# Kernel tuning notes

Measured on AMD Instinct MI355X. Metric: run time of the kernel, lower is better.

The kernel has to match this reference:

```python
import jax, jax.numpy as jnp
import numpy as np

IN_DIM = 256
HID = 256
A = 32          # n_agents
NH = 4          # attention heads
HD = 16         # head_dim = attention_dim / heads
CV = 16         # comm_value_dim
TOPK = 8
NACT = 20
BS = 2048
NEG = -1e10


def _lin(key, out_d, in_d):
    k1, k2 = jax.random.split(key)
    s = 1.0 / np.sqrt(in_d)
    w = jax.random.uniform(k1, (out_d, in_d), jnp.float32, -s, s)
    b = jax.random.uniform(k2, (out_d,), jnp.float32, -s, s)
    return w, b


def setup_inputs() -> dict:
    key = jax.random.key(0)
    ks = jax.random.split(key, 12)
    inputs = jax.random.normal(ks[0], (BS * A, IN_DIM), jnp.float32)
    hidden_state = jax.random.normal(ks[1], (BS * A, HID), jnp.float32)
    fc1_w, fc1_b = _lin(ks[2], HID, IN_DIM)
    gru_w_ih, gru_b_ih = _lin(ks[3], 3 * HID, HID)
    gru_w_hh, gru_b_hh = _lin(ks[4], 3 * HID, HID)
    q_w, q_b = _lin(ks[5], NH * HD, HID)
    k_w, k_b = _lin(ks[6], NH * HD, HID)
    v_w, v_b = _lin(ks[7], NH * CV, HID)
    g_w, g_b = _lin(ks[8], NH, HID)
    p1_w, p1_b = _lin(ks[9], HID, HID + NH * CV)
    p2_w, p2_b = _lin(ks[10], NACT, HID)
    return {
        'inputs': inputs, 'hidden_state': hidden_state,
        'fc1_w': fc1_w, 'fc1_b': fc1_b,
        'gru_w_ih': gru_w_ih, 'gru_w_hh': gru_w_hh,
        'gru_b_ih': gru_b_ih, 'gru_b_hh': gru_b_hh,
        'q_w': q_w, 'q_b': q_b, 'k_w': k_w, 'k_b': k_b,
        'v_w': v_w, 'v_b': v_b, 'g_w': g_w, 'g_b': g_b,
        'p1_w': p1_w, 'p1_b': p1_b, 'p2_w': p2_w, 'p2_b': p2_b,
        'bs': BS,
    }


def _forward(inputs, hidden_state, fc1_w, fc1_b, gru_w_ih, gru_w_hh,
             gru_b_ih, gru_b_hh, q_w, q_b, k_w, k_b, v_w, v_b,
             g_w, g_b, p1_w, p1_b, p2_w, p2_b, bs):
    x = jax.nn.relu(inputs @ fc1_w.T + fc1_b)
    h_in = hidden_state.reshape(-1, HID)
    # torch GRUCell: gates ordered r, z, n
    gi = x @ gru_w_ih.T + gru_b_ih
    gh = h_in @ gru_w_hh.T + gru_b_hh
    gi_r, gi_z, gi_n = jnp.split(gi, 3, axis=-1)
    gh_r, gh_z, gh_n = jnp.split(gh, 3, axis=-1)
    r = jax.nn.sigmoid(gi_r + gh_r)
    z = jax.nn.sigmoid(gi_z + gh_z)
    n = jnp.tanh(gi_n + r * gh_n)
    h = (1.0 - z) * n + z * h_in

    ah = h.reshape(bs, A, HID)                      # agent_hidden
    q = (ah @ q_w.T + q_b).reshape(bs, A, NH, HD)
    k = (ah @ k_w.T + k_b).reshape(bs, A, NH, HD)
    v = (ah @ v_w.T + v_b).reshape(bs, A, NH, CV)

    scores = jnp.einsum('bqhd,bkhd->bqkh', q, k) / np.sqrt(HD)  # [bs,A,A,NH]
    eye = jnp.eye(A, dtype=bool)[None, :, :, None]
    scores = jnp.where(eye, NEG, scores)

    # topk mask along neighbor dim (k < A-1 so mask is applied)
    sp = scores.transpose(0, 1, 3, 2)               # [bs,A,NH,A]
    _, idx = jax.lax.top_k(sp, TOPK)
    keep = jax.nn.one_hot(idx, A, dtype=jnp.float32).sum(axis=-2) > 0
    sp = jnp.where(keep, sp, NEG)
    sparse_scores = sp.transpose(0, 1, 3, 2)        # [bs,A,A,NH]

    alpha = jax.nn.softmax(sparse_scores, axis=2)
    head_messages = jnp.einsum('bqkh,bkhv->bqhv', alpha, v)  # [bs,A,NH,CV]
    gates = jax.nn.sigmoid(ah @ g_w.T + g_b)[..., None]      # [bs,A,NH,1]
    gated = head_messages * gates

    policy_in = jnp.concatenate([ah, gated.reshape(bs, A, NH * CV)], axis=-1)
    policy_in = policy_in.reshape(bs * A, HID + NH * CV)
    logits = jax.nn.relu(policy_in @ p1_w.T + p1_b) @ p2_w.T + p2_b
    return logits, h


def reference(inputs, hidden_state, fc1_w, fc1_b, gru_w_ih, gru_w_hh,
              gru_b_ih, gru_b_hh, q_w, q_b, k_w, k_b, v_w, v_b,
              g_w, g_b, p1_w, p1_b, p2_w, p2_b, bs):
    return _forward(inputs, hidden_state, fc1_w, fc1_b, gru_w_ih, gru_w_hh,
                    gru_b_ih, gru_b_hh, q_w, q_b, k_w, k_b, v_w, v_b,
                    g_w, g_b, p1_w, p1_b, p2_w, p2_b, bs)
```

## Files before the change

### kernel.cpp

```cpp
#include <hip/hip_runtime.h>
#include <hip/hip_bf16.h>
#include <math.h>

#define NBATCH 2048
#define NAG 32
#define HIDD 256
#define INDIM 256
#define PIN 320
#define NACTN 20
#define NEGV -1e10f
#define MT 64
#define NROWS (NBATCH*NAG)

typedef __attribute__((ext_vector_type(8))) __bf16 bf16x8;
typedef __attribute__((ext_vector_type(4))) float f32x4;

#define WO_W1   0
#define WO_WIH  65536
#define WO_WHH  262144
#define WO_WQ   458752
#define WO_WK   475136
#define WO_WV   491520
#define WO_WG   507904
#define WO_WP1  508928
#define WO_WP2  590848
#define WSO_Q   1048576
#define WSO_K   (WSO_Q + NROWS*64)
#define WSO_V   (WSO_K + NROWS*64)
#define WSO_G   (WSO_V + NROWS*64)
#define WSO_MSG (WSO_G + NROWS*4)

__device__ __forceinline__ unsigned short f2bf(float f) {
    union { float f; unsigned int i; } x; x.f = f;
    unsigned int r = x.i + 0x7fffu + ((x.i >> 16) & 1u);
    return (unsigned short)(r >> 16);
}
__device__ __forceinline__ float bf2f(unsigned short u) {
    union { unsigned int i; float f; } x; x.i = ((unsigned int)u) << 16; return x.f;
}
__device__ __forceinline__ float sigm(float x) { return 1.0f / (1.0f + __expf(-x)); }

__device__ __forceinline__ int swz(int row, int col) {
    return row*256 + ((((col >> 3)) ^ (row & 7)) << 3) + (col & 7);
}
__device__ __forceinline__ int swzf(int row, int frag) {
    return row*256 + ((frag ^ (row & 7)) << 3);
}
__device__ __forceinline__ int swzf64(int row, int frag) {
    return row*64 + ((frag ^ (row & 7)) << 3);
}

__device__ __forceinline__ bf16x8 ldfrag(const unsigned short* p) {
    return *(const bf16x8*)(const void*)p;
}
union ZU { uint4 u; bf16x8 v; };
__device__ __forceinline__ bf16x8 zfrag() {
    ZU x; x.u = make_uint4(0u, 0u, 0u, 0u); return x.v;
}
#define MFMA(a,b,c) __builtin_amdgcn_mfma_f32_16x16x32_bf16(a,b,c,0,0,0)

__global__ void __launch_bounds__(256)
convert_weights(const float* __restrict__ W1,  const float* __restrict__ Wih,
                const float* __restrict__ Whh, const float* __restrict__ Wq,
                const float* __restrict__ Wk,  const float* __restrict__ Wv,
                const float* __restrict__ Wg,  const float* __restrict__ Wp1,
                const float* __restrict__ Wp2, unsigned short* __restrict__ dst)
{
    int b = (int)blockIdx.x;
    const float* src; int base;
    if      (b <  64) { src = W1;  base = WO_W1;              }
    else if (b < 256) { src = Wih; base = WO_WIH; b -=  64;   }
    else if (b < 448) { src = Whh; base = WO_WHH; b -= 256;   }
    else if (b < 464) { src = Wq;  base = WO_WQ;  b -= 448;   }
    else if (b < 480) { src = Wk;  base = WO_WK;  b -= 464;   }
    else if (b < 496) { src = Wv;  base = WO_WV;  b -= 480;   }
    else if (b < 497) { src = Wg;  base = WO_WG;  b -= 496;   }
    else if (b < 577) { src = Wp1; base = WO_WP1; b -= 497;   }
    else              { src = Wp2; base = WO_WP2; b -= 577;   }
    const int idx = b * 1024 + (int)threadIdx.x * 4;
    float4 v = *(const float4*)(const void*)(src + idx);
    ushort4 u;
    u.x = f2bf(v.x); u.y = f2bf(v.y); u.z = f2bf(v.z); u.w = f2bf(v.w);
    *(ushort4*)(void*)(dst + base + idx) = u;
}

__global__ void __launch_bounds__(256, 2)
k1_gru_qkvg(const float* __restrict__ gIn, const float* __restrict__ gH,
            const unsigned short* __restrict__ wsW,
            const float* __restrict__ B1,
            const float* __restrict__ Bih, const float* __restrict__ Bhh,
            const float* __restrict__ Bq,  const float* __restrict__ Bk,
            const float* __restrict__ Bv,  const float* __restrict__ Bg,
            float* __restrict__ outH,
            unsigned short* __restrict__ wsQ, unsigned short* __restrict__ wsK,
            unsigned short* __restrict__ wsV, unsigned short* __restrict__ wsG)
{
    __shared__ __align__(16) unsigned short lA[MT*256];
    __shared__ __align__(16) unsigned short lB[MT*256];

    const unsigned short* W1  = wsW + WO_W1;
    const unsigned short* Wih = wsW + WO_WIH;
    const unsigned short* Whh = wsW + WO_WHH;
    const unsigned short* Wq  = wsW + WO_WQ;
    const unsigned short* Wk  = wsW + WO_WK;
    const unsigned short* Wv  = wsW + WO_WV;
    const unsigned short* Wg  = wsW + WO_WG;

    const int tid  = (int)threadIdx.x;
    const int lane = tid & 63;
    const int wv   = tid >> 6;
    const int l15  = lane & 15;
    const int quad = lane >> 4;
    const long rowBase = (long)blockIdx.x * MT;

    #pragma unroll
    for (int i = 0; i < 16; ++i) {
        const int job  = i*256 + tid;
        const int frag = job & 31;
        const int row  = (job >> 5) & 63;
        const int buf  = job >> 11;
        const float* src = (buf ? gH : gIn) + (rowBase + row)*256 + frag*8;
        float4 v0 = *(const float4*)(const void*)(src);
        float4 v1 = *(const float4*)(const void*)(src + 4);
        uint4 pk;
        pk.x = ((unsigned int)f2bf(v0.y) << 16) | f2bf(v0.x);
        pk.y = ((unsigned int)f2bf(v0.w) << 16) | f2bf(v0.z);
        pk.z = ((unsigned int)f2bf(v1.y) << 16) | f2bf(v1.x);
        pk.w = ((unsigned int)f2bf(v1.w) << 16) | f2bf(v1.z);
        unsigned short* dst = buf ? lB : lA;
        *(uint4*)(void*)(dst + swzf(row, frag)) = pk;
    }
    __syncthreads();

    f32x4 xa[4][4];
    #pragma unroll
    for (int i4 = 0; i4 < 4; ++i4) {
        const int nt = i4*4 + wv;
        const int n  = nt*16 + l15;
        f32x4 a0 = {0.f,0.f,0.f,0.f}, a1 = {0.f,0.f,0.f,0.f};
        f32x4 a2 = {0.f,0.f,0.f,0.f}, a3 = {0.f,0.f,0.f,0.f};
        #pragma unroll
        for (int kt = 0; kt < 8; ++kt) {
            const int frag = kt*4 + quad;
            bf16x8 bw = ldfrag(W1 + n*INDIM + frag*8);
            a0 = MFMA(ldfrag(lA + swzf(     l15, frag)), bw, a0);
            a1 = MFMA(ldfrag(lA + swzf(16 + l15, frag)), bw, a1);
            a2 = MFMA(ldfrag(lA + swzf(32 + l15, frag)), bw, a2);
            a3 = MFMA(ldfrag(lA + swzf(48 + l15, frag)), bw, a3);
        }
        const float b = B1[n];
        #pragma unroll
        for (int r = 0; r < 4; ++r) {
            a0[r] = fmaxf(a0[r] + b, 0.f); a1[r] = fmaxf(a1[r] + b, 0.f);
            a2[r] = fmaxf(a2[r] + b, 0.f); a3[r] = fmaxf(a3[r] + b, 0.f);
        }
        xa[i4][0] = a0; xa[i4][1] = a1; xa[i4][2] = a2; xa[i4][3] = a3;
    }
    __syncthreads();
    #pragma unroll
    for (int i4 = 0; i4 < 4; ++i4) {
        const int nt = i4*4 + wv;
        #pragma unroll
        for (int m = 0; m < 4; ++m) {
            #pragma unroll
            for (int r = 0; r < 4; ++r)
                lA[swz(m*16 + quad*4 + r, nt*16 + l15)] = f2bf(xa[i4][m][r]);
        }
    }
    __syncthreads();

    for (int jt = wv; jt < 16; jt += 4) {
        const int n = jt*16 + l15;
        f32x4 ir[4], iz[4], in_[4], hr[4], hz[4], hn[4];
        #pragma unroll
        for (int m = 0; m < 4; ++m) {
            ir[m] = (f32x4){0.f,0.f,0.f,0.f}; iz[m] = (f32x4){0.f,0.f,0.f,0.f};
            in_[m]= (f32x4){0.f,0.f,0.f,0.f}; hr[m] = (f32x4){0.f,0.f,0.f,0.f};
            hz[m] = (f32x4){0.f,0.f,0.f,0.f}; hn[m] = (f32x4){0.f,0.f,0.f,0.f};
        }
        #pragma unroll 2
        for (int kt = 0; kt < 8; ++kt) {
            const int frag = kt*4 + quad;
            const int k0 = frag*8;
            bf16x8 ax[4], ah[4];
            #pragma unroll
            for (int m = 0; m < 4; ++m) {
                ax[m] = ldfrag(lA + swzf(m*16 + l15, frag));
                ah[m] = ldfrag(lB + swzf(m*16 + l15, frag));
            }
            bf16x8 br = ldfrag(Wih + (n      )*HIDD + k0);
            bf16x8 bz = ldfrag(Wih + (n + 256)*HIDD + k0);
            bf16x8 bn = ldfrag(Wih + (n + 512)*HIDD + k0);
            bf16x8 cr = ldfrag(Whh + (n      )*HIDD + k0);
            bf16x8 cz = ldfrag(Whh + (n + 256)*HIDD + k0);
            bf16x8 cn = ldfrag(Whh + (n + 512)*HIDD + k0);
            #pragma unroll
            for (int m = 0; m < 4; ++m) {
                ir[m] = MFMA(ax[m], br, ir[m]);
                iz[m] = MFMA(ax[m], bz, iz[m]);
                in_[m]= MFMA(ax[m], bn, in_[m]);
                hr[m] = MFMA(ah[m], cr, hr[m]);
                hz[m] = MFMA(ah[m], cz, hz[m]);
                hn[m] = MFMA(ah[m], cn, hn[m]);
            }
        }
        const float bir_ = Bih[n], biz_ = Bih[n+256], bin_ = Bih[n+512];
        const float bhr_ = Bhh[n], bhz_ = Bhh[n+256], bhn_ = Bhh[n+512];
        #pragma unroll
        for (int m = 0; m < 4; ++m) {
            #pragma unroll
            for (int r = 0; r < 4; ++r) {
                const int row = m*16 + quad*4 + r;
                const float hprev = bf2f(lB[swz(row, n)]);
                const float rr = sigm(ir[m][r] + bir_ + hr[m][r] + bhr_);
                const float zz = sigm(iz[m][r] + biz_ + hz[m][r] + bhz_);
                const float nn = tanhf(in_[m][r] + bin_ + rr*(hn[m][r] + bhn_));
                outH[(rowBase + row)*HIDD + n] = (1.0f - zz)*nn + zz*hprev;
            }
        }
    }
    __syncthreads();

    #pragma unroll
    for (int i = 0; i < 8; ++i) {
        const int job  = i*256 + tid;
        const int frag = job & 31;
        const int row  = job >> 5;
        const float* src = outH + (rowBase + row)*256 + frag*8;
        float4 v0 = *(const float4*)(const void*)(src);
        float4 v1 = *(const float4*)(const void*)(src + 4);
        uint4 pk;
        pk.x = ((unsigned int)f2bf(v0.y) << 16) | f2bf(v0.x);
        pk.y = ((unsigned int)f2bf(v0.w) << 16) | f2bf(v0.z);
        pk.z = ((unsigned int)f2bf(v1.y) << 16) | f2bf(v1.x);
        pk.w = ((unsigned int)f2bf(v1.w) << 16) | f2bf(v1.z);
        *(uint4*)(void*)(lA + swzf(row, frag)) = pk;
    }
    __syncthreads();

    for (int job = wv; job < 13; job += 4) {
        const unsigned short* W; const float* Bi; unsigned short* dst; int nb;
        if      (job < 4)  { W = Wq; Bi = Bq; dst = wsQ; nb = job;     }
        else if (job < 8)  { W = Wk; Bi = Bk; dst = wsK; nb = job - 4; }
        else if (job < 12) { W = Wv; Bi = Bv; dst = wsV; nb = job - 8; }
        else               { W = Wg; Bi = Bg; dst = wsG; nb = 0;       }
        const bool isg   = (job == 12);
        const bool valid = !isg || (l15 < 4);
        const int n = nb*16 + l15;
        f32x4 ac[4];
        #pragma unroll
        for (int m = 0; m < 4; ++m) ac[m] = (f32x4){0.f,0.f,0.f,0.f};
        #pragma unroll
        for (int kt = 0; kt < 8; ++kt) {
            const int frag = kt*4 + quad;
            bf16x8 bw = valid ? ldfrag(W + n*HIDD + frag*8) : zfrag();
            #pragma unroll
            for (int m = 0; m < 4; ++m)
                ac[m] = MFMA(ldfrag(lA + swzf(m*16 + l15, frag)), bw, ac[m]);
        }
        if (valid) {
            const float b = Bi[n];
            #pragma unroll
            for (int m = 0; m < 4; ++m) {
                #pragma unroll
                for (int r = 0; r < 4; ++r) {
                    const int row = m*16 + quad*4 + r;
                    const float v = ac[m][r] + b;
                    if (isg) dst[(rowBase + row)*4  + l15]          = f2bf(v);
                    else     dst[(rowBase + row)*64 + nb*16 + l15]  = f2bf(v);
                }
            }
        }
    }
}

#define QS 68
__global__ void __launch_bounds__(256, 4)
k2_attn(const unsigned short* __restrict__ wsQ, const unsigned short* __restrict__ wsK,
        const unsigned short* __restrict__ wsV, const unsigned short* __restrict__ wsG,
        unsigned short* __restrict__ wsM)
{
    __shared__ unsigned short sQ[2][32*QS];
    __shared__ unsigned short sK[2][32*QS];
    __shared__ unsigned short sV[2][32*QS];
    __shared__ unsigned short sG[2][32*4];

    const int tid = (int)threadIdx.x;
    const long b0 = (long)blockIdx.x * 2;

    #pragma unroll
    for (int i = 0; i < 12; ++i) {
        const int j  = i*256 + tid;
        const int b  = (j >= 1536) ? 1 : 0;
        const int jj = b ? (j - 1536) : j;
        const int mat = jj >> 9;
        const int e   = jj & 511;
        const int row = e >> 4, c4 = e & 15;
        const unsigned short* srcm = (mat == 0) ? wsQ : (mat == 1) ? wsK : wsV;
        unsigned short* dstm = (mat == 0) ? sQ[b] : (mat == 1) ? sK[b] : sV[b];
        *(ushort4*)(void*)(dstm + row*QS + c4*4) =
            *(const ushort4*)(const void*)(srcm + ((b0 + b)*32 + row)*64 + c4*4);
    }
    if (tid < 64) {
        const int b = tid >> 5, row = tid & 31;
        *(ushort4*)(void*)(sG[b] + row*4) =
            *(const ushort4*)(const void*)(wsG + ((b0 + b)*32 + row)*4);
    }
    __syncthreads();

    const int b  = tid >> 7;
    const int h  = (tid >> 5) & 3;
    const int qi = tid & 31;
    const unsigned short* q_ = sQ[b];
    const unsigned short* k_ = sK[b];
    const unsigned short* v_ = sV[b];

    float qv[16];
    #pragma unroll
    for (int c = 0; c < 16; ++c) qv[c] = bf2f(q_[qi*QS + h*16 + c]);
    float s0[32];
    #pragma unroll
    for (int ki = 0; ki < 32; ++ki) {
        float acc = 0.0f;
        #pragma unroll
        for (int c = 0; c < 16; ++c) acc += qv[c] * bf2f(k_[ki*QS + h*16 + c]);
        acc *= 0.25f;
        s0[ki] = (ki == qi) ? NEGV : acc;
    }
    unsigned int mask = 0u;
    float m1 = 0.0f;
    for (int t = 0; t < 8; ++t) {
        float best = -3.0e38f; int bidx = 0;
        #pragma unroll
        for (int i = 0; i < 32; ++i) {
            bool better = (((mask >> i) & 1u) == 0u) && (s0[i] > best);
            best = better ? s0[i] : best;
            bidx = better ? i : bidx;
        }
        mask |= (1u << bidx);
        if (t == 0) m1 = best;
    }
    float sum = 0.0f;
    #pragma unroll
    for (int i = 0; i < 32; ++i) {
        float v = ((mask >> i) & 1u) ? s0[i] : NEGV;
        sum += __expf(v - m1);
    }
    const float inv = 1.0f / sum;
    const float gate = sigm(bf2f(sG[b][qi*4 + h]));
    float msg[16];
    #pragma unroll
    for (int c = 0; c < 16; ++c) msg[c] = 0.0f;
    #pragma unroll
    for (int ki = 0; ki < 32; ++ki) {
        float v = ((mask >> ki) & 1u) ? s0[ki] : NEGV;
        float al = __expf(v - m1) * inv;
        #pragma unroll
        for (int c = 0; c < 16; ++c) msg[c] += al * bf2f(v_[ki*QS + h*16 + c]);
    }
    unsigned short mb[16];
    #pragma unroll
    for (int c = 0; c < 16; ++c) mb[c] = f2bf(msg[c] * gate);
    unsigned short* dst = wsM + ((b0 + b)*32 + qi)*64 + h*16;
    #pragma unroll
    for (int c4 = 0; c4 < 4; ++c4) {
        ushort4 u;
        u.x = mb[c4*4]; u.y = mb[c4*4+1]; u.z = mb[c4*4+2]; u.w = mb[c4*4+3];
        *(ushort4*)(void*)(dst + c4*4) = u;
    }
}

__global__ void __launch_bounds__(256, 3)
k3_policy(const float* __restrict__ gHnew, const unsigned short* __restrict__ wsW,
          const unsigned short* __restrict__ wsM,
          const float* __restrict__ Bp1, const float* __restrict__ Bp2,
          float* __restrict__ outL)
{
    __shared__ __align__(16) unsigned short lH[MT*256];
    __shared__ __align__(16) unsigned short lM[MT*64];

    const unsigned short* Wp1 = wsW + WO_WP1;
    const unsigned short* Wp2 = wsW + WO_WP2;

    const int tid  = (int)threadIdx.x;
    const int lane = tid & 63;
    const int wv   = tid >> 6;
    const int l15  = lane & 15;
    const int quad = lane >> 4;
    const long rowBase = (long)blockIdx.x * MT;

    #pragma unroll
    for (int i = 0; i < 8; ++i) {
        const int job  = i*256 + tid;
        const int frag = job & 31;
        const int row  = job >> 5;
        const float* src = gHnew + (rowBase + row)*256 + frag*8;
        float4 v0 = *(const float4*)(const void*)(src);
        float4 v1 = *(const float4*)(const void*)(src + 4);
        uint4 pk;
        pk.x = ((unsigned int)f2bf(v0.y) << 16) | f2bf(v0.x);
        pk.y = ((unsigned int)f2bf(v0.w) << 16) | f2bf(v0.z);
        pk.z = ((unsigned int)f2bf(v1.y) << 16) | f2bf(v1.x);
        pk.w = ((unsigned int)f2bf(v1.w) << 16) | f2bf(v1.z);
        *(uint4*)(void*)(lH + swzf(row, frag)) = pk;
    }
    #pragma unroll
    for (int i = 0; i < 2; ++i) {
        const int job  = i*256 + tid;
        const int frag = job & 7;
        const int row  = job >> 3;
        *(uint4*)(void*)(lM + swzf64(row, frag)) =
            *(const uint4*)(const void*)(wsM + (rowBase + row)*64 + frag*8);
    }
    __syncthreads();

    f32x4 pa[4][4];
    #pragma unroll
    for (int i4 = 0; i4 < 4; ++i4) {
        const int nt = i4*4 + wv;
        const int n  = nt*16 + l15;
        f32x4 a0 = {0.f,0.f,0.f,0.f}, a1 = {0.f,0.f,0.f,0.f};
        f32x4 a2 = {0.f,0.f,0.f,0.f}, a3 = {0.f,0.f,0.f,0.f};
        #pragma unroll
        for (int kt = 0; kt < 10; ++kt) {
            bf16x8 bw = ldfrag(Wp1 + n*PIN + kt*32 + quad*8);
            bf16x8 f0, f1, f2, f3;
            if (kt < 8) {
                const int frag = kt*4 + quad;
                f0 = ldfrag(lH + swzf(     l15, frag));
                f1 = ldfrag(lH + swzf(16 + l15, frag));
                f2 = ldfrag(lH + swzf(32 + l15, frag));
                f3 = ldfrag(lH + swzf(48 + l15, frag));
            } else {
                const int frag = (kt - 8)*4 + quad;
                f0 = ldfrag(lM + swzf64(     l15, frag));
                f1 = ldfrag(lM + swzf64(16 + l15, frag));
                f2 = ldfrag(lM + swzf64(32 + l15, frag));
                f3 = ldfrag(lM + swzf64(48 + l15, frag));
            }
            a0 = MFMA(f0, bw, a0); a1 = MFMA(f1, bw, a1);
            a2 = MFMA(f2, bw, a2); a3 = MFMA(f3, bw, a3);
        }
        const float b = Bp1[n];
        #pragma unroll
        for (int r = 0; r < 4; ++r) {
            a0[r] = fmaxf(a0[r] + b, 0.f); a1[r] = fmaxf(a1[r] + b, 0.f);
            a2[r] = fmaxf(a2[r] + b, 0.f); a3[r] = fmaxf(a3[r] + b, 0.f);
        }
        pa[i4][0] = a0; pa[i4][1] = a1; pa[i4][2] = a2; pa[i4][3] = a3;
    }
    __syncthreads();
    #pragma unroll
    for (int i4 = 0; i4 < 4; ++i4) {
        const int nt = i4*4 + wv;
        #pragma unroll
        for (int m = 0; m < 4; ++m) {
            #pragma unroll
            for (int r = 0; r < 4; ++r)
                lH[swz(m*16 + quad*4 + r, nt*16 + l15)] = f2bf(pa[i4][m][r]);
        }
    }
    __syncthreads();

    for (int j = wv; j < 8; j += 4) {
        const int ntile = j >> 2, m = j & 3;
        const int n = ntile*16 + l15;
        const bool valid = (n < NACTN);
        f32x4 ac = {0.f,0.f,0.f,0.f};
        #pragma unroll
        for (int kt = 0; kt < 8; ++kt) {
            const int frag = kt*4 + quad;
            bf16x8 bw = valid ? ldfrag(Wp2 + n*HIDD + frag*8) : zfrag();
            ac = MFMA(ldfrag(lH + swzf(m*16 + l15, frag)), bw, ac);
        }
        if (valid) {
            const float b = Bp2[n];
            #pragma unroll
            for (int r = 0; r < 4; ++r)
                outL[(rowBase + m*16 + quad*4 + r)*NACTN + n] = ac[r] + b;
        }
    }
}

extern "C" void kernel_launch(void* const* d_in, const int* in_sizes, int n_in,
                              void* d_out, int out_size, void* d_ws, size_t ws_size,
                              hipStream_t stream) {
    (void)in_sizes; (void)n_in; (void)ws_size; (void)out_size;
    const float* gIn = (const float*)d_in[0];
    const float* gH  = (const float*)d_in[1];
    const float* W1  = (const float*)d_in[2];
    const float* B1  = (const float*)d_in[3];
    const float* Wih = (const float*)d_in[4];
    const float* Whh = (const float*)d_in[5];
    const float* Bih = (const float*)d_in[6];
    const float* Bhh = (const float*)d_in[7];
    const float* Wq  = (const float*)d_in[8];
    const float* Bq  = (const float*)d_in[9];
    const float* Wk  = (const float*)d_in[10];
    const float* Bk  = (const float*)d_in[11];
    const float* Wv  = (const float*)d_in[12];
    const float* Bv  = (const float*)d_in[13];
    const float* Wg  = (const float*)d_in[14];
    const float* Bg  = (const float*)d_in[15];
    const float* Wp1 = (const float*)d_in[16];
    const float* Bp1 = (const float*)d_in[17];
    const float* Wp2 = (const float*)d_in[18];
    const float* Bp2 = (const float*)d_in[19];
    float* outL = (float*)d_out;
    float* outH = outL + (size_t)NBATCH * NAG * NACTN;
    unsigned short* wsW = (unsigned short*)d_ws;

    hipLaunchKernelGGL(convert_weights, dim3(582), dim3(256), 0, stream,
        W1, Wih, Whh, Wq, Wk, Wv, Wg, Wp1, Wp2, wsW);
    hipLaunchKernelGGL(k1_gru_qkvg, dim3(NROWS/MT), dim3(256), 0, stream,
        gIn, gH, wsW, B1, Bih, Bhh, Bq, Bk, Bv, Bg,
        outH, wsW + WSO_Q, wsW + WSO_K, wsW + WSO_V, wsW + WSO_G);
    hipLaunchKernelGGL(k2_attn, dim3(NBATCH/2), dim3(256), 0, stream,
        wsW + WSO_Q, wsW + WSO_K, wsW + WSO_V, wsW + WSO_G, wsW + WSO_MSG);
    hipLaunchKernelGGL(k3_policy, dim3(NROWS/MT), dim3(256), 0, stream,
        outH, wsW, wsW + WSO_MSG, Bp1, Bp2, outL);
}
```

Measured before the change: 414.2 us.

## Pre-convert hidden state to bf16 and restructure GRU kernel for higher occupancy

Adds a kernel that converts the incoming hidden state to bf16 in workspace. A new GRU kernel uses a single LDS buffer, reads the bf16 h_prev straight from global memory, and writes a bf16 copy of the new h for the policy kernel to load without conversion. This lets the GRU kernel target 4 blocks per CU instead of 2, and the policy kernel's occupancy hint is also raised. Separately, sigmoid and tanh now use a fast reciprocal, and the attention softmax caches its exponentials so they are not recomputed. The new path runs only when the workspace is large enough. It adds an extra pass over the hidden state plus additional workspace traffic.

```diff
diff --git a/kernel.cpp b/kernel.cpp
--- a/kernel.cpp
+++ b/kernel.cpp
@@ -29,6 +29,9 @@
 #define WSO_V   (WSO_K + NROWS*64)
 #define WSO_G   (WSO_V + NROWS*64)
 #define WSO_MSG (WSO_G + NROWS*4)
+#define WSO_H   (WSO_MSG + NROWS*64)
+#define WSO_HO  (WSO_H + NROWS*256)
+#define WS_NEED_BYTES ((size_t)(WSO_HO + (size_t)NROWS*256) * 2u)
 
 __device__ __forceinline__ unsigned short f2bf(float f) {
     union { float f; unsigned int i; } x; x.f = f;
@@ -38,7 +41,12 @@
 __device__ __forceinline__ float bf2f(unsigned short u) {
     union { unsigned int i; float f; } x; x.i = ((unsigned int)u) << 16; return x.f;
 }
-__device__ __forceinline__ float sigm(float x) { return 1.0f / (1.0f + __expf(-x)); }
+__device__ __forceinline__ float frcp(float x) { return __builtin_amdgcn_rcpf(x); }
+__device__ __forceinline__ float sigm(float x) { return frcp(1.0f + __expf(-x)); }
+__device__ __forceinline__ float tanh_fast(float x) {
+    float e = __expf(2.0f * x);
+    return 1.0f - 2.0f * frcp(e + 1.0f);
+}
 
 __device__ __forceinline__ int swz(int row, int col) {
     return row*256 + ((((col >> 3)) ^ (row & 7)) << 3) + (col & 7);
@@ -84,16 +92,223 @@
     *(ushort4*)(void*)(dst + base + idx) = u;
 }
 
+__global__ void __launch_bounds__(256)
+convert_h(const float* __restrict__ gH, unsigned short* __restrict__ wsHO)
+{
+    const long base = (long)blockIdx.x * 16384;
+    const int tid = (int)threadIdx.x;
+    #pragma unroll
+    for (int i = 0; i < 8; ++i) {
+        const long off = base + (long)(i*256 + tid) * 8;
+        float4 v0 = *(const float4*)(const void*)(gH + off);
+        float4 v1 = *(const float4*)(const void*)(gH + off + 4);
+        uint4 pk;
+        pk.x = ((unsigned int)f2bf(v0.y) << 16) | f2bf(v0.x);
+        pk.y = ((unsigned int)f2bf(v0.w) << 16) | f2bf(v0.z);
+        pk.z = ((unsigned int)f2bf(v1.y) << 16) | f2bf(v1.x);
+        pk.w = ((unsigned int)f2bf(v1.w) << 16) | f2bf(v1.z);
+        *(uint4*)(void*)(wsHO + off) = pk;
+    }
+}
+
+__global__ void __launch_bounds__(256, 4)
+k1_new(const float* __restrict__ gIn,
+       const unsigned short* __restrict__ wsW,
+       const unsigned short* __restrict__ wsHO,
+       const float* __restrict__ B1,
+       const float* __restrict__ Bih, const float* __restrict__ Bhh,
+       const float* __restrict__ Bq,  const float* __restrict__ Bk,
+       const float* __restrict__ Bv,  const float* __restrict__ Bg,
+       float* __restrict__ outH, unsigned short* __restrict__ wsH,
+       unsigned short* __restrict__ wsQ, unsigned short* __restrict__ wsK,
+       unsigned short* __restrict__ wsV, unsigned short* __restrict__ wsG)
+{
+    __shared__ __align__(16) unsigned short lA[MT*256];
+
+    const unsigned short* W1  = wsW + WO_W1;
+    const unsigned short* Wih = wsW + WO_WIH;
+    const unsigned short* Whh = wsW + WO_WHH;
+    const unsigned short* Wq  = wsW + WO_WQ;
+    const unsigned short* Wk  = wsW + WO_WK;
+    const unsigned short* Wv  = wsW + WO_WV;
+    const unsigned short* Wg  = wsW + WO_WG;
+
+    const int tid  = (int)threadIdx.x;
+    const int lane = tid & 63;
+    const int wv   = tid >> 6;
+    const int l15  = lane & 15;
+    const int quad = lane >> 4;
+    const long rowBase = (long)blockIdx.x * MT;
+
+    #pragma unroll
+    for (int i = 0; i < 8; ++i) {
+        const int job  = i*256 + tid;
+        const int frag = job & 31;
+        const int row  = job >> 5;
+        const float* src = gIn + (rowBase + row)*256 + frag*8;
+        float4 v0 = *(const float4*)(const void*)(src);
+        float4 v1 = *(const float4*)(const void*)(src + 4);
+        uint4 pk;
+        pk.x = ((unsigned int)f2bf(v0.y) << 16) | f2bf(v0.x);
+        pk.y = ((unsigned int)f2bf(v0.w) << 16) | f2bf(v0.z);
+        pk.z = ((unsigned int)f2bf(v1.y) << 16) | f2bf(v1.x);
+        pk.w = ((unsigned int)f2bf(v1.w) << 16) | f2bf(v1.z);
+        *(uint4*)(void*)(lA + swzf(row, frag)) = pk;
+    }
+    __syncthreads();
+
+    f32x4 xa[4][4];
+    #pragma unroll
+    for (int i4 = 0; i4 < 4; ++i4) {
+        const int nt = i4*4 + wv;
+        const int n  = nt*16 + l15;
+        f32x4 a0 = {0.f,0.f,0.f,0.f}, a1 = {0.f,0.f,0.f,0.f};
+        f32x4 a2 = {0.f,0.f,0.f,0.f}, a3 = {0.f,0.f,0.f,0.f};
+        #pragma unroll
+        for (int kt = 0; kt < 8; ++kt) {
+            const int frag = kt*4 + quad;
+            bf16x8 bw = ldfrag(W1 + n*INDIM + frag*8);
+            a0 = MFMA(ldfrag(lA + swzf(     l15, frag)), bw, a0);
+            a1 = MFMA(ldfrag(lA + swzf(16 + l15, frag)), bw, a1);
+            a2 = MFMA(ldfrag(lA + swzf(32 + l15, frag)), bw, a2);
+            a3 = MFMA(ldfrag(lA + swzf(48 + l15, frag)), bw, a3);
+        }
+        const float b = B1[n];
+        #pragma unroll
+        for (int r = 0; r < 4; ++r) {
+            a0[r] = fmaxf(a0[r] + b, 0.f); a1[r] = fmaxf(a1[r] + b, 0.f);
+            a2[r] = fmaxf(a2[r] + b, 0.f); a3[r] = fmaxf(a3[r] + b, 0.f);
+        }
+        xa[i4][0] = a0; xa[i4][1] = a1; xa[i4][2] = a2; xa[i4][3] = a3;
+    }
+    __syncthreads();
+    #pragma unroll
+    for (int i4 = 0; i4 < 4; ++i4) {
+        const int nt = i4*4 + wv;
+        #pragma unroll
+        for (int m = 0; m < 4; ++m) {
+            #pragma unroll
+            for (int r = 0; r < 4; ++r)
+                lA[swz(m*16 + quad*4 + r, nt*16 + l15)] = f2bf(xa[i4][m][r]);
+        }
+    }
+    __syncthreads();
+
+    for (int jt = wv; jt < 16; jt += 4) {
+        const int n = jt*16 + l15;
+        const float bir_ = Bih[n], biz_ = Bih[n+256], bin_ = Bih[n+512];
+        const float bhr_ = Bhh[n], bhz_ = Bhh[n+256], bhn_ = Bhh[n+512];
+        #pragma unroll
+        for (int half = 0; half < 2; ++half) {
+            const int r0 = half*32;
+            f32x4 ir0={0.f,0.f,0.f,0.f}, ir1={0.f,0.f,0.f,0.f};
+            f32x4 iz0={0.f,0.f,0.f,0.f}, iz1={0.f,0.f,0.f,0.f};
+            f32x4 in0={0.f,0.f,0.f,0.f}, in1={0.f,0.f,0.f,0.f};
+            f32x4 hr0={0.f,0.f,0.f,0.f}, hr1={0.f,0.f,0.f,0.f};
+            f32x4 hz0={0.f,0.f,0.f,0.f}, hz1={0.f,0.f,0.f,0.f};
+            f32x4 hn0={0.f,0.f,0.f,0.f}, hn1={0.f,0.f,0.f,0.f};
+            #pragma unroll 2
+            for (int kt = 0; kt < 8; ++kt) {
+                const int frag = kt*4 + quad;
+                const int k0 = frag*8;
+                bf16x8 ax0 = ldfrag(lA + swzf(r0 +      l15, frag));
+                bf16x8 ax1 = ldfrag(lA + swzf(r0 + 16 + l15, frag));
+                bf16x8 ah0 = ldfrag(wsHO + (rowBase + r0 +      l15)*256 + k0);
+                bf16x8 ah1 = ldfrag(wsHO + (rowBase + r0 + 16 + l15)*256 + k0);
+                bf16x8 br = ldfrag(Wih + (n      )*HIDD + k0);
+                bf16x8 bz = ldfrag(Wih + (n + 256)*HIDD + k0);
+                bf16x8 bn = ldfrag(Wih + (n + 512)*HIDD + k0);
+                bf16x8 cr = ldfrag(Whh + (n      )*HIDD + k0);
+                bf16x8 cz = ldfrag(Whh + (n + 256)*HIDD + k0);
+                bf16x8 cn = ldfrag(Whh + (n + 512)*HIDD + k0);
+                ir0 = MFMA(ax0, br, ir0); ir1 = MFMA(ax1, br, ir1);
+                iz0 = MFMA(ax0, bz, iz0); iz1 = MFMA(ax1, bz, iz1);
+                in0 = MFMA(ax0, bn, in0); in1 = MFMA(ax1, bn, in1);
+                hr0 = MFMA(ah0, cr, hr0); hr1 = MFMA(ah1, cr, hr1);
+                hz0 = MFMA(ah0, cz, hz0); hz1 = MFMA(ah1, cz, hz1);
+                hn0 = MFMA(ah0, cn, hn0); hn1 = MFMA(ah1, cn, hn1);
+            }
+            #pragma unroll
+            for (int mm = 0; mm < 2; ++mm) {
+                f32x4 gr = mm ? ir1 : ir0;
+                f32x4 gz = mm ? iz1 : iz0;
+                f32x4 gn = mm ? in1 : in0;
+                f32x4 hr_ = mm ? hr1 : hr0;
+                f32x4 hz_ = mm ? hz1 : hz0;
+                f32x4 hn_ = mm ? hn1 : hn0;
+                #pragma unroll
+                for (int r = 0; r < 4; ++r) {
+                    const int rw = r0 + mm*16 + quad*4 + r;
+                    const long go = (rowBase + rw)*256 + n;
+                    const float hprev = bf2f(wsHO[go]);
+                    const float rr = sigm(gr[r] + bir_ + hr_[r] + bhr_);
+                    const float zz = sigm(gz[r] + biz_ + hz_[r] + bhz_);
+                    const float nn = tanh_fast(gn[r] + bin_ + rr*(hn_[r] + bhn_));
+                    const float hv = (1.0f - zz)*nn + zz*hprev;
+                    outH[go] = hv;
+                    wsH[go]  = f2bf(hv);
+                }
+            }
+        }
+    }
+    __syncthreads();
+
+    #pragma unroll
+    for (int i = 0; i < 8; ++i) {
+        const int job  = i*256 + tid;
+        const int frag = job & 31;
+        const int row  = job >> 5;
+        *(uint4*)(void*)(lA + swzf(row, frag)) =
+            *(const uint4*)(const void*)(wsH + (rowBase + row)*256 + frag*8);
+    }
+    __syncthreads();
+
+    for (int job = wv; job < 13; job += 4) {
+        const unsigned short* W; const float* Bi; unsigned short* dst; int nb;
+        if      (job < 4)  { W = Wq; Bi = Bq; dst = wsQ; nb = job;     }
+        else if (job < 8)  { W = Wk; Bi = Bk; dst = wsK; nb = job - 4; }
+        else if (job < 12) { W = Wv; Bi = Bv; dst = wsV; nb = job - 8; }
+        else               { W = Wg; Bi = Bg; dst = wsG; nb = 0;       }
+        const bool isg   = (job == 12);
+        const bool valid = !isg || (l15 < 4);
+        const int n = nb*16 + l15;
+        f32x4 ac[4];
+        #pragma unroll
+        for (int m = 0; m < 4; ++m) ac[m] = (f32x4){0.f,0.f,0.f,0.f};
+        #pragma unroll
+        for (int kt = 0; kt < 8; ++kt) {
+            const int frag = kt*4 + quad;
+            bf16x8 bw = valid ? ldfrag(W + n*HIDD + frag*8) : zfrag();
+            #pragma unroll
+            for (int m = 0; m < 4; ++m)
+                ac[m] = MFMA(ldfrag(lA + swzf(m*16 + l15, frag)), bw, ac[m]);
+        }
+        if (valid) {
+            const float b = Bi[n];
+            #pragma unroll
+            for (int m = 0; m < 4; ++m) {
+                #pragma unroll
+                for (int r = 0; r < 4; ++r) {
+                    const int row = m*16 + quad*4 + r;
+                    const float v = ac[m][r] + b;
+                    if (isg) dst[(rowBase + row)*4  + l15]          = f2bf(v);
+                    else     dst[(rowBase + row)*64 + nb*16 + l15]  = f2bf(v);
+                }
+            }
+        }
+    }
+}
+
 __global__ void __launch_bounds__(256, 2)
-k1_gru_qkvg(const float* __restrict__ gIn, const float* __restrict__ gH,
-            const unsigned short* __restrict__ wsW,
-            const float* __restrict__ B1,
-            const float* __restrict__ Bih, const float* __restrict__ Bhh,
-            const float* __restrict__ Bq,  const float* __restrict__ Bk,
-            const float* __restrict__ Bv,  const float* __restrict__ Bg,
-            float* __restrict__ outH,
-            unsigned short* __restrict__ wsQ, unsigned short* __restrict__ wsK,
-            unsigned short* __restrict__ wsV, unsigned short* __restrict__ wsG)
+k1_fb(const float* __restrict__ gIn, const float* __restrict__ gH,
+      const unsigned short* __restrict__ wsW,
+      const float* __restrict__ B1,
+      const float* __restrict__ Bih, const float* __restrict__ Bhh,
+      const float* __restrict__ Bq,  const float* __restrict__ Bk,
+      const float* __restrict__ Bv,  const float* __restrict__ Bg,
+      float* __restrict__ outH,
+      unsigned short* __restrict__ wsQ, unsigned short* __restrict__ wsK,
+      unsigned short* __restrict__ wsV, unsigned short* __restrict__ wsG)
 {
     __shared__ __align__(16) unsigned short lA[MT*256];
     __shared__ __align__(16) unsigned short lB[MT*256];
@@ -214,7 +429,7 @@
                 const float hprev = bf2f(lB[swz(row, n)]);
                 const float rr = sigm(ir[m][r] + bir_ + hr[m][r] + bhr_);
                 const float zz = sigm(iz[m][r] + biz_ + hz[m][r] + bhz_);
-                const float nn = tanhf(in_[m][r] + bin_ + rr*(hn[m][r] + bhn_));
+                const float nn = tanh_fast(in_[m][r] + bin_ + rr*(hn[m][r] + bhn_));
                 outH[(rowBase + row)*HIDD + n] = (1.0f - zz)*nn + zz*hprev;
             }
         }
@@ -343,18 +558,18 @@
     float sum = 0.0f;
     #pragma unroll
     for (int i = 0; i < 32; ++i) {
-        float v = ((mask >> i) & 1u) ? s0[i] : NEGV;
-        sum += __expf(v - m1);
-    }
-    const float inv = 1.0f / sum;
+        const float e = ((mask >> i) & 1u) ? __expf(s0[i] - m1) : 0.0f;
+        s0[i] = e;
+        sum += e;
+    }
+    const float inv = frcp(sum);
     const float gate = sigm(bf2f(sG[b][qi*4 + h]));
     float msg[16];
     #pragma unroll
     for (int c = 0; c < 16; ++c) msg[c] = 0.0f;
     #pragma unroll
     for (int ki = 0; ki < 32; ++ki) {
-        float v = ((mask >> ki) & 1u) ? s0[ki] : NEGV;
-        float al = __expf(v - m1) * inv;
+        const float al = s0[ki] * inv;
         #pragma unroll
         for (int c = 0; c < 16; ++c) msg[c] += al * bf2f(v_[ki*QS + h*16 + c]);
     }
@@ -370,11 +585,11 @@
     }
 }
 
-__global__ void __launch_bounds__(256, 3)
+__global__ void __launch_bounds__(256, 4)
 k3_policy(const float* __restrict__ gHnew, const unsigned short* __restrict__ wsW,
-          const unsigned short* __restrict__ wsM,
+          const unsigned short* __restrict__ wsM, const unsigned short* __restrict__ wsH,
           const float* __restrict__ Bp1, const float* __restrict__ Bp2,
-          float* __restrict__ outL)
+          float* __restrict__ outL, int useH16)
 {
     __shared__ __align__(16) unsigned short lH[MT*256];
     __shared__ __align__(16) unsigned short lM[MT*64];
@@ -389,20 +604,31 @@
     const int quad = lane >> 4;
     const long rowBase = (long)blockIdx.x * MT;
 
-    #pragma unroll
-    for (int i = 0; i < 8; ++i) {
-        const int job  = i*256 + tid;
-        const int frag = job & 31;
-        const int row  = job >> 5;
-        const float* src = gHnew + (rowBase + row)*256 + frag*8;
-        float4 v0 = *(const float4*)(const void*)(src);
-        float4 v1 = *(const float4*)(const void*)(src + 4);
-        uint4 pk;
-        pk.x = ((unsigned int)f2bf(v0.y) << 16) | f2bf(v0.x);
-        pk.y = ((unsigned int)f2bf(v0.w) << 16) | f2bf(v0.z);
-        pk.z = ((unsigned int)f2bf(v1.y) << 16) | f2bf(v1.x);
-        pk.w = ((unsigned int)f2bf(v1.w) << 16) | f2bf(v1.z);
-        *(uint4*)(void*)(lH + swzf(row, frag)) = pk;
+    if (useH16) {
+        #pragma unroll
+        for (int i = 0; i < 8; ++i) {
+            const int job  = i*256 + tid;
+            const int frag = job & 31;
+            const int row  = job >> 5;
+            *(uint4*)(void*)(lH + swzf(row, frag)) =
+                *(const uint4*)(const void*)(wsH + (rowBase + row)*256 + frag*8);
+        }
+    } else {
+        #pragma unroll
+        for (int i = 0; i < 8; ++i) {
+            const int job  = i*256 + tid;
+            const int frag = job & 31;
+            const int row  = job >> 5;
+            const float* src = gHnew + (rowBase + row)*256 + frag*8;
+            float4 v0 = *(const float4*)(const void*)(src);
+            float4 v1 = *(const float4*)(const void*)(src + 4);
+            uint4 pk;
+            pk.x = ((unsigned int)f2bf(v0.y) << 16) | f2bf(v0.x);
+            pk.y = ((unsigned int)f2bf(v0.w) << 16) | f2bf(v0.z);
+            pk.z = ((unsigned int)f2bf(v1.y) << 16) | f2bf(v1.x);
+            pk.w = ((unsigned int)f2bf(v1.w) << 16) | f2bf(v1.z);
+            *(uint4*)(void*)(lH + swzf(row, frag)) = pk;
+        }
     }
     #pragma unroll
     for (int i = 0; i < 2; ++i) {
@@ -485,7 +711,7 @@
 extern "C" void kernel_launch(void* const* d_in, const int* in_sizes, int n_in,
                               void* d_out, int out_size, void* d_ws, size_t ws_size,
                               hipStream_t stream) {
-    (void)in_sizes; (void)n_in; (void)ws_size; (void)out_size;
+    (void)in_sizes; (void)n_in; (void)out_size;
     const float* gIn = (const float*)d_in[0];
     const float* gH  = (const float*)d_in[1];
     const float* W1  = (const float*)d_in[2];
@@ -510,13 +736,24 @@
     float* outH = outL + (size_t)NBATCH * NAG * NACTN;
     unsigned short* wsW = (unsigned short*)d_ws;
 
+    const int preconv = (ws_size >= WS_NEED_BYTES) ? 1 : 0;
+
     hipLaunchKernelGGL(convert_weights, dim3(582), dim3(256), 0, stream,
         W1, Wih, Whh, Wq, Wk, Wv, Wg, Wp1, Wp2, wsW);
-    hipLaunchKernelGGL(k1_gru_qkvg, dim3(NROWS/MT), dim3(256), 0, stream,
-        gIn, gH, wsW, B1, Bih, Bhh, Bq, Bk, Bv, Bg,
-        outH, wsW + WSO_Q, wsW + WSO_K, wsW + WSO_V, wsW + WSO_G);
+    if (preconv) {
+        hipLaunchKernelGGL(convert_h, dim3(1024), dim3(256), 0, stream,
+            gH, wsW + WSO_HO);
+        hipLaunchKernelGGL(k1_new, dim3(NROWS/MT), dim3(256), 0, stream,
+            gIn, wsW, wsW + WSO_HO, B1, Bih, Bhh, Bq, Bk, Bv, Bg,
+            outH, wsW + WSO_H,
+            wsW + WSO_Q, wsW + WSO_K, wsW + WSO_V, wsW + WSO_G);
+    } else {
+        hipLaunchKernelGGL(k1_fb, dim3(NROWS/MT), dim3(256), 0, stream,
+            gIn, gH, wsW, B1, Bih, Bhh, Bq, Bk, Bv, Bg,
+            outH, wsW + WSO_Q, wsW + WSO_K, wsW + WSO_V, wsW + WSO_G);
+    }
     hipLaunchKernelGGL(k2_attn, dim3(NBATCH/2), dim3(256), 0, stream,
         wsW + WSO_Q, wsW + WSO_K, wsW + WSO_V, wsW + WSO_G, wsW + WSO_MSG);
     hipLaunchKernelGGL(k3_policy, dim3(NROWS/MT), dim3(256), 0, stream,
-        outH, wsW, wsW + WSO_MSG, Bp1, Bp2, outL);
-}
+        outH, wsW, wsW + WSO_MSG, wsW + WSO_H, Bp1, Bp2, outL, preconv);
+}
```

Result: slower. 656.0 us (+58.4%).

## Fuse attention kernel into policy kernel and use fast sigmoid/tanh

Applied to the files above, without the earlier changes.

Merges the top-k sparse attention kernel into the policy MLP kernel. Each 64-row block now computes the gated messages for its two batches straight into shared memory, so the message workspace round trip through global memory and one launch go away. The hidden layer is written to a separate LDS buffer, which removes the register staging and the extra barrier. It also swaps in hardware reciprocal for sigmoid and an exp-based tanh in the GRU epilogue, at some cost in precision. Extra LDS use and a lower occupancy bound (2 blocks) are the tradeoff.

```diff
diff --git a/kernel.cpp b/kernel.cpp
--- a/kernel.cpp
+++ b/kernel.cpp
@@ -28,7 +28,6 @@
 #define WSO_K   (WSO_Q + NROWS*64)
 #define WSO_V   (WSO_K + NROWS*64)
 #define WSO_G   (WSO_V + NROWS*64)
-#define WSO_MSG (WSO_G + NROWS*4)
 
 __device__ __forceinline__ unsigned short f2bf(float f) {
     union { float f; unsigned int i; } x; x.f = f;
@@ -38,13 +37,21 @@
 __device__ __forceinline__ float bf2f(unsigned short u) {
     union { unsigned int i; float f; } x; x.i = ((unsigned int)u) << 16; return x.f;
 }
-__device__ __forceinline__ float sigm(float x) { return 1.0f / (1.0f + __expf(-x)); }
+__device__ __forceinline__ float frcp(float x) { return __builtin_amdgcn_rcpf(x); }
+__device__ __forceinline__ float sigm(float x) { return frcp(1.0f + __expf(-x)); }
+__device__ __forceinline__ float tanh_fast(float x) {
+    float e = __expf(2.0f * x);
+    return 1.0f - 2.0f * frcp(e + 1.0f);
+}
 
 __device__ __forceinline__ int swz(int row, int col) {
     return row*256 + ((((col >> 3)) ^ (row & 7)) << 3) + (col & 7);
 }
 __device__ __forceinline__ int swzf(int row, int frag) {
     return row*256 + ((frag ^ (row & 7)) << 3);
+}
+__device__ __forceinline__ int swz64(int row, int col) {
+    return row*64 + ((((col >> 3)) ^ (row & 7)) << 3) + (col & 7);
 }
 __device__ __forceinline__ int swzf64(int row, int frag) {
     return row*64 + ((frag ^ (row & 7)) << 3);
@@ -214,7 +221,7 @@
                 const float hprev = bf2f(lB[swz(row, n)]);
                 const float rr = sigm(ir[m][r] + bir_ + hr[m][r] + bhr_);
                 const float zz = sigm(iz[m][r] + biz_ + hz[m][r] + bhz_);
-                const float nn = tanhf(in_[m][r] + bin_ + rr*(hn[m][r] + bhn_));
+                const float nn = tanh_fast(in_[m][r] + bin_ + rr*(hn[m][r] + bhn_));
                 outH[(rowBase + row)*HIDD + n] = (1.0f - zz)*nn + zz*hprev;
             }
         }
@@ -275,109 +282,20 @@
 }
 
 #define QS 68
-__global__ void __launch_bounds__(256, 4)
-k2_attn(const unsigned short* __restrict__ wsQ, const unsigned short* __restrict__ wsK,
-        const unsigned short* __restrict__ wsV, const unsigned short* __restrict__ wsG,
-        unsigned short* __restrict__ wsM)
-{
-    __shared__ unsigned short sQ[2][32*QS];
-    __shared__ unsigned short sK[2][32*QS];
-    __shared__ unsigned short sV[2][32*QS];
-    __shared__ unsigned short sG[2][32*4];
-
-    const int tid = (int)threadIdx.x;
-    const long b0 = (long)blockIdx.x * 2;
-
-    #pragma unroll
-    for (int i = 0; i < 12; ++i) {
-        const int j  = i*256 + tid;
-        const int b  = (j >= 1536) ? 1 : 0;
-        const int jj = b ? (j - 1536) : j;
-        const int mat = jj >> 9;
-        const int e   = jj & 511;
-        const int row = e >> 4, c4 = e & 15;
-        const unsigned short* srcm = (mat == 0) ? wsQ : (mat == 1) ? wsK : wsV;
-        unsigned short* dstm = (mat == 0) ? sQ[b] : (mat == 1) ? sK[b] : sV[b];
-        *(ushort4*)(void*)(dstm + row*QS + c4*4) =
-            *(const ushort4*)(const void*)(srcm + ((b0 + b)*32 + row)*64 + c4*4);
-    }
-    if (tid < 64) {
-        const int b = tid >> 5, row = tid & 31;
-        *(ushort4*)(void*)(sG[b] + row*4) =
-            *(const ushort4*)(const void*)(wsG + ((b0 + b)*32 + row)*4);
-    }
-    __syncthreads();
-
-    const int b  = tid >> 7;
-    const int h  = (tid >> 5) & 3;
-    const int qi = tid & 31;
-    const unsigned short* q_ = sQ[b];
-    const unsigned short* k_ = sK[b];
-    const unsigned short* v_ = sV[b];
-
-    float qv[16];
-    #pragma unroll
-    for (int c = 0; c < 16; ++c) qv[c] = bf2f(q_[qi*QS + h*16 + c]);
-    float s0[32];
-    #pragma unroll
-    for (int ki = 0; ki < 32; ++ki) {
-        float acc = 0.0f;
-        #pragma unroll
-        for (int c = 0; c < 16; ++c) acc += qv[c] * bf2f(k_[ki*QS + h*16 + c]);
-        acc *= 0.25f;
-        s0[ki] = (ki == qi) ? NEGV : acc;
-    }
-    unsigned int mask = 0u;
-    float m1 = 0.0f;
-    for (int t = 0; t < 8; ++t) {
-        float best = -3.0e38f; int bidx = 0;
-        #pragma unroll
-        for (int i = 0; i < 32; ++i) {
-            bool better = (((mask >> i) & 1u) == 0u) && (s0[i] > best);
-            best = better ? s0[i] : best;
-            bidx = better ? i : bidx;
-        }
-        mask |= (1u << bidx);
-        if (t == 0) m1 = best;
-    }
-    float sum = 0.0f;
-    #pragma unroll
-    for (int i = 0; i < 32; ++i) {
-        float v = ((mask >> i) & 1u) ? s0[i] : NEGV;
-        sum += __expf(v - m1);
-    }
-    const float inv = 1.0f / sum;
-    const float gate = sigm(bf2f(sG[b][qi*4 + h]));
-    float msg[16];
-    #pragma unroll
-    for (int c = 0; c < 16; ++c) msg[c] = 0.0f;
-    #pragma unroll
-    for (int ki = 0; ki < 32; ++ki) {
-        float v = ((mask >> ki) & 1u) ? s0[ki] : NEGV;
-        float al = __expf(v - m1) * inv;
-        #pragma unroll
-        for (int c = 0; c < 16; ++c) msg[c] += al * bf2f(v_[ki*QS + h*16 + c]);
-    }
-    unsigned short mb[16];
-    #pragma unroll
-    for (int c = 0; c < 16; ++c) mb[c] = f2bf(msg[c] * gate);
-    unsigned short* dst = wsM + ((b0 + b)*32 + qi)*64 + h*16;
-    #pragma unroll
-    for (int c4 = 0; c4 < 4; ++c4) {
-        ushort4 u;
-        u.x = mb[c4*4]; u.y = mb[c4*4+1]; u.z = mb[c4*4+2]; u.w = mb[c4*4+3];
-        *(ushort4*)(void*)(dst + c4*4) = u;
-    }
-}
-
-__global__ void __launch_bounds__(256, 3)
-k3_policy(const float* __restrict__ gHnew, const unsigned short* __restrict__ wsW,
-          const unsigned short* __restrict__ wsM,
-          const float* __restrict__ Bp1, const float* __restrict__ Bp2,
-          float* __restrict__ outL)
+__global__ void __launch_bounds__(256, 2)
+k23_attn_policy(const float* __restrict__ gHnew,
+                const unsigned short* __restrict__ wsW,
+                const unsigned short* __restrict__ wsQ,
+                const unsigned short* __restrict__ wsK,
+                const unsigned short* __restrict__ wsV,
+                const unsigned short* __restrict__ wsG,
+                const float* __restrict__ Bp1, const float* __restrict__ Bp2,
+                float* __restrict__ outL)
 {
     __shared__ __align__(16) unsigned short lH[MT*256];
+    __shared__ __align__(16) unsigned short lP[MT*256];
     __shared__ __align__(16) unsigned short lM[MT*64];
+    __shared__ __align__(16) unsigned short sG[2*32*4];
 
     const unsigned short* Wp1 = wsW + WO_WP1;
     const unsigned short* Wp2 = wsW + WO_WP2;
@@ -388,6 +306,7 @@
     const int l15  = lane & 15;
     const int quad = lane >> 4;
     const long rowBase = (long)blockIdx.x * MT;
+    const long b0 = (long)blockIdx.x * 2;
 
     #pragma unroll
     for (int i = 0; i < 8; ++i) {
@@ -405,16 +324,82 @@
         *(uint4*)(void*)(lH + swzf(row, frag)) = pk;
     }
     #pragma unroll
-    for (int i = 0; i < 2; ++i) {
-        const int job  = i*256 + tid;
-        const int frag = job & 7;
-        const int row  = job >> 3;
-        *(uint4*)(void*)(lM + swzf64(row, frag)) =
-            *(const uint4*)(const void*)(wsM + (rowBase + row)*64 + frag*8);
-    }
-    __syncthreads();
-
-    f32x4 pa[4][4];
+    for (int i = 0; i < 12; ++i) {
+        const int j  = i*256 + tid;
+        const int b  = (j >= 1536) ? 1 : 0;
+        const int jj = b ? (j - 1536) : j;
+        const int mat = jj >> 9;
+        const int e   = jj & 511;
+        const int row = e >> 4, c4 = e & 15;
+        const unsigned short* srcm = (mat == 0) ? wsQ : (mat == 1) ? wsK : wsV;
+        *(ushort4*)(void*)(lP + ((b*3 + mat)*32 + row)*QS + c4*4) =
+            *(const ushort4*)(const void*)(srcm + ((b0 + b)*32 + row)*64 + c4*4);
+    }
+    if (tid < 64) {
+        const int b = tid >> 5, row = tid & 31;
+        *(ushort4*)(void*)(sG + (b*32 + row)*4) =
+            *(const ushort4*)(const void*)(wsG + ((b0 + b)*32 + row)*4);
+    }
+    __syncthreads();
+
+    {
+        const int b  = tid >> 7;
+        const int h  = (tid >> 5) & 3;
+        const int qi = tid & 31;
+        const unsigned short* q_ = lP + (b*3 + 0)*32*QS;
+        const unsigned short* k_ = lP + (b*3 + 1)*32*QS;
+        const unsigned short* v_ = lP + (b*3 + 2)*32*QS;
+
+        float qv[16];
+        #pragma unroll
+        for (int c = 0; c < 16; ++c) qv[c] = bf2f(q_[qi*QS + h*16 + c]);
+        float s0[32];
+        #pragma unroll
+        for (int ki = 0; ki < 32; ++ki) {
+            float acc = 0.0f;
+            #pragma unroll
+            for (int c = 0; c < 16; ++c) acc += qv[c] * bf2f(k_[ki*QS + h*16 + c]);
+            acc *= 0.25f;
+            s0[ki] = (ki == qi) ? NEGV : acc;
+        }
+        unsigned int mask = 0u;
+        float m1 = 0.0f;
+        for (int t = 0; t < 8; ++t) {
+            float best = -3.0e38f; int bidx = 0;
+            #pragma unroll
+            for (int i = 0; i < 32; ++i) {
+                bool better = (((mask >> i) & 1u) == 0u) && (s0[i] > best);
+                best = better ? s0[i] : best;
+                bidx = better ? i : bidx;
+            }
+            mask |= (1u << bidx);
+            if (t == 0) m1 = best;
+        }
+        float sum = 0.0f;
+        #pragma unroll
+        for (int i = 0; i < 32; ++i) {
+            const float e = ((mask >> i) & 1u) ? __expf(s0[i] - m1) : 0.0f;
+            s0[i] = e;
+            sum += e;
+        }
+        const float inv = frcp(sum);
+        const float gate = sigm(bf2f(sG[(b*32 + qi)*4 + h]));
+        float msg[16];
+        #pragma unroll
+        for (int c = 0; c < 16; ++c) msg[c] = 0.0f;
+        #pragma unroll
+        for (int ki = 0; ki < 32; ++ki) {
+            const float al = s0[ki] * inv;
+            #pragma unroll
+            for (int c = 0; c < 16; ++c) msg[c] += al * bf2f(v_[ki*QS + h*16 + c]);
+        }
+        const int mrow = b*32 + qi;
+        #pragma unroll
+        for (int c = 0; c < 16; ++c)
+            lM[swz64(mrow, h*16 + c)] = f2bf(msg[c] * gate);
+    }
+    __syncthreads();
+
     #pragma unroll
     for (int i4 = 0; i4 < 4; ++i4) {
         const int nt = i4*4 + wv;
@@ -444,20 +429,10 @@
         const float b = Bp1[n];
         #pragma unroll
         for (int r = 0; r < 4; ++r) {
-            a0[r] = fmaxf(a0[r] + b, 0.f); a1[r] = fmaxf(a1[r] + b, 0.f);
-            a2[r] = fmaxf(a2[r] + b, 0.f); a3[r] = fmaxf(a3[r] + b, 0.f);
-        }
-        pa[i4][0] = a0; pa[i4][1] = a1; pa[i4][2] = a2; pa[i4][3] = a3;
-    }
-    __syncthreads();
-    #pragma unroll
-    for (int i4 = 0; i4 < 4; ++i4) {
-        const int nt = i4*4 + wv;
-        #pragma unroll
-        for (int m = 0; m < 4; ++m) {
-            #pragma unroll
-            for (int r = 0; r < 4; ++r)
-                lH[swz(m*16 + quad*4 + r, nt*16 + l15)] = f2bf(pa[i4][m][r]);
+            lP[swz(     quad*4 + r, n)] = f2bf(fmaxf(a0[r] + b, 0.f));
+            lP[swz(16 + quad*4 + r, n)] = f2bf(fmaxf(a1[r] + b, 0.f));
+            lP[swz(32 + quad*4 + r, n)] = f2bf(fmaxf(a2[r] + b, 0.f));
+            lP[swz(48 + quad*4 + r, n)] = f2bf(fmaxf(a3[r] + b, 0.f));
         }
     }
     __syncthreads();
@@ -471,7 +446,7 @@
         for (int kt = 0; kt < 8; ++kt) {
             const int frag = kt*4 + quad;
             bf16x8 bw = valid ? ldfrag(Wp2 + n*HIDD + frag*8) : zfrag();
-            ac = MFMA(ldfrag(lH + swzf(m*16 + l15, frag)), bw, ac);
+            ac = MFMA(ldfrag(lP + swzf(m*16 + l15, frag)), bw, ac);
         }
         if (valid) {
             const float b = Bp2[n];
@@ -515,8 +490,7 @@
     hipLaunchKernelGGL(k1_gru_qkvg, dim3(NROWS/MT), dim3(256), 0, stream,
         gIn, gH, wsW, B1, Bih, Bhh, Bq, Bk, Bv, Bg,
         outH, wsW + WSO_Q, wsW + WSO_K, wsW + WSO_V, wsW + WSO_G);
-    hipLaunchKernelGGL(k2_attn, dim3(NBATCH/2), dim3(256), 0, stream,
-        wsW + WSO_Q, wsW + WSO_K, wsW + WSO_V, wsW + WSO_G, wsW + WSO_MSG);
-    hipLaunchKernelGGL(k3_policy, dim3(NROWS/MT), dim3(256), 0, stream,
-        outH, wsW, wsW + WSO_MSG, Bp1, Bp2, outL);
-}
+    hipLaunchKernelGGL(k23_attn_policy, dim3(NROWS/MT), dim3(256), 0, stream,
+        outH, wsW, wsW + WSO_Q, wsW + WSO_K, wsW + WSO_V, wsW + WSO_G,
+        Bp1, Bp2, outL);
+}
```

New measurement: 398.3 us. 1.04x faster.
